# Kernel optimization log

Measured on AMD Instinct MI355X. Metric: run time of the kernel, lower is better.

## Reference

```python
import jax, jax.numpy as jnp
from jax import lax
import numpy as np

KS = 5
STRIDE = 4
SCALE = 10.0
PAD = 1        # conv_transpose2d padding (hardcoded in source)
OUT_PAD = 1    # output_padding
DN = ('NCHW', 'OIHW', 'NCHW')


def _same_pad(x, ks, stride):
    # torch same_padding: pad so out = ceil(H/stride)
    H, W = x.shape[-2], x.shape[-1]
    oh = -(-H // stride); ow = -(-W // stride)
    ph = max(0, (oh - 1) * stride + ks - H)
    pw = max(0, (ow - 1) * stride + ks - W)
    return jnp.pad(x, ((0, 0), (0, 0), (ph // 2, ph - ph // 2), (pw // 2, pw - pw // 2)))


def _patches(x, ks, stride):
    # torch extract_image_patches (same padding + unfold), returned as [N, L, C, ks, ks]
    N, C, H, W = x.shape
    oh = -(-H // stride); ow = -(-W // stride)
    xp = _same_pad(x, ks, stride)
    ys = (jnp.arange(oh) * stride)[:, None] + jnp.arange(ks)[None, :]   # [oh, ks]
    xs = (jnp.arange(ow) * stride)[:, None] + jnp.arange(ks)[None, :]   # [ow, ks]
    p = xp[:, :, ys, :][:, :, :, :, xs]   # [N, C, oh, ks, ow, ks]
    return p.transpose(0, 2, 4, 1, 3, 5).reshape(N, oh * ow, C, ks, ks)


def _conv3(x, W, b):
    # BasicBlock: 3x3 conv pad 1 + bias + LeakyReLU(0.01)
    y = lax.conv_general_dilated(x, W, (1, 1), [(1, 1), (1, 1)], dimension_numbers=DN)
    return jax.nn.leaky_relu(y + b[None, :, None, None], 0.01)


def _attend(qp, kp, vp):
    # qp: [C, Hp, Wp] padded query feature; kp: [L, C, ks, ks]; vp: [L, B, ks, ks]
    kmax = jnp.max(jnp.sqrt(jnp.sum(kp * kp, axis=(1, 2, 3))))
    kn = kp / kmax
    w = lax.conv_general_dilated(qp[None], kn, (STRIDE, STRIDE), 'VALID', dimension_numbers=DN)  # [1, L, h, w]
    wn = jax.nn.softmax(w * SCALE, axis=1)
    # conv_transpose2d(wn, vp, stride=4, padding=1, output_padding=1) as lhs-dilated conv
    ker = jnp.flip(vp.transpose(1, 0, 2, 3), (2, 3))  # [B, L, ks, ks]
    lo = KS - 1 - PAD
    hi = KS - 1 - PAD + OUT_PAD
    out = lax.conv_general_dilated(wn, ker, (1, 1), [(lo, hi), (lo, hi)],
                                   lhs_dilation=(STRIDE, STRIDE), dimension_numbers=DN)
    return out[0] / 6.0


def setup_inputs() -> dict:
    key = jax.random.key(0)
    k = jax.random.split(key, 12)
    N, CIN, MID, B = 8, 64, 64, 64
    H, HL = 256, 64
    s = 0.05
    return {
        'ms':   jax.random.normal(k[0], (N, B, HL, HL), jnp.float32),
        'pan':  jax.random.normal(k[1], (N, CIN, H, H), jnp.float32),
        'pan2': jax.random.normal(k[2], (N, CIN, HL, HL), jnp.float32),
        'Wq': jax.random.normal(k[3], (MID, CIN, 3, 3), jnp.float32) * s,
        'bq': jnp.zeros((MID,), jnp.float32),
        'Wk': jax.random.normal(k[4], (MID, CIN, 3, 3), jnp.float32) * s,
        'bk': jnp.zeros((MID,), jnp.float32),
        'Wv': jax.random.normal(k[5], (B, B, 3, 3), jnp.float32) * s,
        'bv': jnp.zeros((B,), jnp.float32),
        'Wr': jax.random.normal(k[6], (B, B, 3, 3), jnp.float32) * s,
        'br': jnp.zeros((B,), jnp.float32),
    }


def reference(ms, pan, pan2, Wq, bq, Wk, bk, Wv, bv, Wr, br):
    k_fea = _conv3(pan2, Wk, bk)               # [N, MID, 64, 64]
    k_patch = _patches(k_fea, KS, STRIDE)      # [N, L=256, MID, 5, 5]
    q_fea = _conv3(pan, Wq, bq)                # [N, MID, 256, 256]
    q_pad = _same_pad(q_fea, KS, STRIDE)       # [N, MID, 257, 257]
    v_fea = _conv3(ms, Wv, bv)                 # [N, B, 64, 64]
    v_patch = _patches(v_fea, KS, STRIDE)      # [N, L, B, 5, 5]
    res = jax.vmap(_attend)(q_pad, k_patch, v_patch)  # [N, B, 256, 256]
    return _conv3(res, Wr, br)
```

## Files before the change

### kernel.cpp

```cpp
#include <hip/hip_runtime.h>
#include <math.h>

#define NB   8
#define CI   64
#define COC  64
#define HQ   256
#define HK   64
#define KS   5
#define LL   256
#define NPAD 1664
#define QP2  (257 * 264)

typedef __attribute__((ext_vector_type(8))) short bf16x8s;
typedef __attribute__((ext_vector_type(4))) float f32x4;

static __device__ __forceinline__ unsigned short f2bf(float f) {
  union { float f; unsigned u; } v; v.f = f;
  unsigned r = v.u + 0x7FFF + ((v.u >> 16) & 1);
  return (unsigned short)(r >> 16);
}
static __device__ __forceinline__ float bf2f(unsigned short h) {
  union { unsigned u; float f; } v; v.u = ((unsigned)h) << 16; return v.f;
}

__global__ void wtrans_mfma(const float* __restrict__ Wt, unsigned short* __restrict__ wimg) {
  const int ch = blockIdx.x;
  const int tap = ch >> 1, cih = ch & 1;
  for (int idx = threadIdx.x; idx < 64 * 40; idx += 256) {
    const int co = idx / 40, s = idx - co * 40;
    unsigned short v = 0;
    if (s < 32) v = f2bf(Wt[((size_t)co * 64 + cih * 32 + s) * 9 + tap]);
    wimg[(size_t)ch * 64 * 40 + idx] = v;
  }
}

__global__ void pad_rci(const float* __restrict__ src, unsigned short* __restrict__ dst) {
  const int ct = blockIdx.x, g = blockIdx.y, n = blockIdx.z;
  const int c0 = ct * 66;
  __shared__ float t[64 * 68];
  const int jl = threadIdx.x & 63, cg = threadIdx.x >> 6;
  const int row = g - 1;
  const bool rok = (row >= 0 && row < 256);
  for (int ci = cg; ci < 64; ci += 4) {
    #pragma unroll
    for (int jb = 0; jb < 2; ++jb) {
      const int j = jl + jb * 64;
      if (j < 66) {
        const int x = c0 - 1 + j;
        float v = 0.f;
        if (rok && x >= 0 && x < 256)
          v = src[(((size_t)n * 64 + ci) * 256 + row) * 256 + x];
        t[ci * 68 + j] = v;
      }
    }
  }
  __syncthreads();
  const int cil = threadIdx.x & 63, cc = threadIdx.x >> 6;
  unsigned short* db = dst + (((size_t)n * 258 + g) * 264) * 64;
  for (int c = cc; c < 66; c += 4)
    db[(size_t)(c0 + c) * 64 + cil] = f2bf(t[cil * 68 + c]);
}

__global__ void pad_rci_s(const float* __restrict__ src, unsigned short* __restrict__ dst) {
  const int g = blockIdx.x;
  const int n = blockIdx.y;
  __shared__ float t[64 * 68];
  const int jl = threadIdx.x & 63, cg = threadIdx.x >> 6;
  const int row = g - 1;
  const bool rok = (row >= 0 && row < 64);
  for (int ci = cg; ci < 64; ci += 4) {
    #pragma unroll
    for (int jb = 0; jb < 2; ++jb) {
      const int j = jl + jb * 64;
      if (j < 66) {
        const int x = j - 1;
        float v = 0.f;
        if (rok && x >= 0 && x < 64)
          v = src[(((size_t)n * 64 + ci) * 64 + row) * 64 + x];
        t[ci * 68 + j] = v;
      }
    }
  }
  __syncthreads();
  const int cil = threadIdx.x & 63, cc = threadIdx.x >> 6;
  unsigned short* db = dst + ((size_t)n * 66 + g) * 72 * 64;
  for (int c = cc; c < 66; c += 4)
    db[(size_t)c * 64 + cil] = f2bf(t[cil * 68 + c]);
}

__global__ void rbz(unsigned short* __restrict__ resbf) {
  const int n = blockIdx.x;
  unsigned short* b = resbf + (size_t)n * 258 * 264 * 64;
  for (int idx = threadIdx.x; idx < 264 * 64; idx += 256) {
    b[idx] = 0;
    b[(size_t)257 * 264 * 64 + idx] = 0;
  }
  for (int idx = threadIdx.x; idx < 256 * 64; idx += 256) {
    const int r = idx >> 6, ci = idx & 63;
    b[((size_t)(r + 1) * 264) * 64 + ci] = 0;
    b[((size_t)(r + 1) * 264 + 257) * 64 + ci] = 0;
  }
}

__global__ void qz(unsigned short* __restrict__ qhi, unsigned short* __restrict__ qlo) {
  const int n = blockIdx.x;
  unsigned short* bh = qhi + (size_t)n * QP2 * 64;
  unsigned short* bl = qlo + (size_t)n * QP2 * 64;
  for (int g = threadIdx.x; g < 4224; g += 256) {
    ((unsigned long long*)(bh + (size_t)256 * 264 * 64))[g] = 0ull;
    ((unsigned long long*)(bl + (size_t)256 * 264 * 64))[g] = 0ull;
  }
  for (int g = threadIdx.x; g < 4096; g += 256) {
    const int r = g >> 4, q = g & 15;
    const size_t off = ((size_t)r * 264 + 256) * 64 + q * 4;
    *(unsigned long long*)(bh + off) = 0ull;
    *(unsigned long long*)(bl + off) = 0ull;
  }
}

__global__ __launch_bounds__(256) void conv3m(
    const unsigned short* __restrict__ inbf,
    const unsigned short* __restrict__ wimg,
    const float* __restrict__ bias,
    float* __restrict__ out, int PS, int RS, int inRS, long long inIS) {
  const int x0 = blockIdx.x * 64;
  const int y0 = blockIdx.y * 2;
  const int n  = blockIdx.z;
  const int tid = threadIdx.x;
  const int lane = tid & 63;
  const int wv = tid >> 6;
  const int col = lane & 15;
  const int kg  = lane >> 4;

  __shared__ unsigned short in_s[4 * 66 * 72];

  {
    const unsigned short* src = inbf + (size_t)n * inIS + (size_t)y0 * inRS;
    for (int pos = tid; pos < 264; pos += 256) {
      const int r = pos / 66, c = pos - r * 66;
      const unsigned short* s = src + (size_t)r * inRS + (size_t)(x0 + c) * 64;
      unsigned short* d = &in_s[pos * 72];
      #pragma unroll
      for (int q = 0; q < 8; ++q)
        *(float4*)(d + q * 8) = *(const float4*)(s + q * 8);
    }
  }
  __syncthreads();

  f32x4 acc[2][4];
  #pragma unroll
  for (int ry = 0; ry < 2; ++ry)
    #pragma unroll
    for (int p = 0; p < 4; ++p) acc[ry][p] = (f32x4){0.f, 0.f, 0.f, 0.f};

  const unsigned short* wbase = wimg + ((size_t)(wv * 16 + col)) * 40 + kg * 8;

  for (int ch = 0; ch < 18; ++ch) {
    const int tap = ch >> 1, cih = ch & 1;
    const int dy = tap / 3, dx = tap - dy * 3;
    const bf16x8s a = *(const bf16x8s*)(wbase + (size_t)ch * 64 * 40);
    const int cix = cih * 32 + kg * 8;
    #pragma unroll
    for (int ry = 0; ry < 2; ++ry)
      #pragma unroll
      for (int p = 0; p < 4; ++p) {
        const int c = p * 16 + col + dx;
        const bf16x8s b = *(const bf16x8s*)&in_s[((ry + dy) * 66 + c) * 72 + cix];
        acc[ry][p] = __builtin_amdgcn_mfma_f32_16x16x32_bf16(a, b, acc[ry][p], 0, 0, 0);
      }
  }

  const int cobase = wv * 16 + kg * 4;
  const float4 bb = *(const float4*)&bias[cobase];
  const float bv[4] = {bb.x, bb.y, bb.z, bb.w};
  #pragma unroll
  for (int ry = 0; ry < 2; ++ry)
    #pragma unroll
    for (int p = 0; p < 4; ++p) {
      const int x = x0 + p * 16 + col;
      #pragma unroll
      for (int r = 0; r < 4; ++r) {
        float t = acc[ry][p][r] + bv[r];
        t = t > 0.f ? t : 0.01f * t;
        out[(size_t)(n * 64 + cobase + r) * PS + (size_t)(y0 + ry) * RS + x] = t;
      }
    }
}

__global__ __launch_bounds__(256) void conv3mq(
    const unsigned short* __restrict__ inbf,
    const unsigned short* __restrict__ wimg,
    const float* __restrict__ bias,
    unsigned short* __restrict__ qhi, unsigned short* __restrict__ qlo) {
  const int x0 = blockIdx.x * 64;
  const int y0 = blockIdx.y * 2;
  const int n  = blockIdx.z;
  const int tid = threadIdx.x;
  const int lane = tid & 63;
  const int wv = tid >> 6;
  const int col = lane & 15;
  const int kg  = lane >> 4;

  __shared__ unsigned short in_s[4 * 66 * 72];

  {
    const unsigned short* src = inbf + ((size_t)n * 258 + y0) * 264 * 64;
    for (int pos = tid; pos < 264; pos += 256) {
      const int r = pos / 66, c = pos - r * 66;
      const unsigned short* s = src + ((size_t)r * 264 + x0 + c) * 64;
      unsigned short* d = &in_s[pos * 72];
      #pragma unroll
      for (int q = 0; q < 8; ++q)
        *(float4*)(d + q * 8) = *(const float4*)(s + q * 8);
    }
  }
  __syncthreads();

  f32x4 acc[2][4];
  #pragma unroll
  for (int ry = 0; ry < 2; ++ry)
    #pragma unroll
    for (int p = 0; p < 4; ++p) acc[ry][p] = (f32x4){0.f, 0.f, 0.f, 0.f};

  const unsigned short* wbase = wimg + ((size_t)(wv * 16 + col)) * 40 + kg * 8;

  for (int ch = 0; ch < 18; ++ch) {
    const int tap = ch >> 1, cih = ch & 1;
    const int dy = tap / 3, dx = tap - dy * 3;
    const bf16x8s a = *(const bf16x8s*)(wbase + (size_t)ch * 64 * 40);
    const int cix = cih * 32 + kg * 8;
    #pragma unroll
    for (int ry = 0; ry < 2; ++ry)
      #pragma unroll
      for (int p = 0; p < 4; ++p) {
        const int c = p * 16 + col + dx;
        const bf16x8s b = *(const bf16x8s*)&in_s[((ry + dy) * 66 + c) * 72 + cix];
        acc[ry][p] = __builtin_amdgcn_mfma_f32_16x16x32_bf16(a, b, acc[ry][p], 0, 0, 0);
      }
  }

  const int cobase = wv * 16 + kg * 4;
  const float4 bb = *(const float4*)&bias[cobase];
  const float bv[4] = {bb.x, bb.y, bb.z, bb.w};
  #pragma unroll
  for (int ry = 0; ry < 2; ++ry) {
    unsigned short* hb = qhi + ((size_t)n * 257 + (y0 + ry)) * 264 * 64;
    unsigned short* lb = qlo + ((size_t)n * 257 + (y0 + ry)) * 264 * 64;
    #pragma unroll
    for (int p = 0; p < 4; ++p) {
      const int x = x0 + p * 16 + col;
      unsigned long long hp = 0, lp = 0;
      #pragma unroll
      for (int r = 0; r < 4; ++r) {
        float t = acc[ry][p][r] + bv[r];
        t = t > 0.f ? t : 0.01f * t;
        const unsigned short h = f2bf(t);
        const unsigned short lo = f2bf(t - bf2f(h));
        hp |= ((unsigned long long)h) << (16 * r);
        lp |= ((unsigned long long)lo) << (16 * r);
      }
      *(unsigned long long*)(hb + (size_t)x * 64 + cobase) = hp;
      *(unsigned long long*)(lb + (size_t)x * 64 + cobase) = lp;
    }
  }
}

__global__ void knorm_kernel(const float* __restrict__ kfea, float* __restrict__ norms) {
  const int l = blockIdx.x, n = blockIdx.y, c = threadIdx.x;
  const int ly = l >> 4, lx = l & 15;
  const float* base = kfea + ((size_t)(n * CI + c) * HK) * HK;
  float ss = 0.f;
  #pragma unroll
  for (int i = 0; i < KS; ++i) {
    const int r = 4 * ly + i;
    if (r >= HK) continue;
    #pragma unroll
    for (int j = 0; j < KS; ++j) {
      const int cc = 4 * lx + j;
      if (cc >= HK) continue;
      const float v = base[r * HK + cc];
      ss = fmaf(v, v, ss);
    }
  }
  for (int off = 32; off; off >>= 1) ss += __shfl_down(ss, off);
  if (c == 0) norms[n * LL + l] = ss;
}

__global__ void kscale_kernel(const float* __restrict__ norms, float* __restrict__ kscale) {
  const int n = blockIdx.x, t = threadIdx.x;
  float v = norms[n * LL + t];
  for (int off = 32; off; off >>= 1) v = fmaxf(v, __shfl_down(v, off));
  __shared__ float red[4];
  if ((t & 63) == 0) red[t >> 6] = v;
  __syncthreads();
  if (t == 0) {
    const float m = fmaxf(fmaxf(red[0], red[1]), fmaxf(red[2], red[3]));
    kscale[n] = 10.0f / sqrtf(m);
  }
}

__global__ void kp_gather2(const float* __restrict__ kfea, const float* __restrict__ kscale,
                           unsigned short* __restrict__ khi, unsigned short* __restrict__ klo) {
  const int tap = blockIdx.x, cih = blockIdx.y, n = blockIdx.z;
  const int s = threadIdx.x & 31, lg = threadIdx.x >> 5;
  const int i = tap / 5, j = tap % 5;
  const float sc = kscale[n];
  const float* kb = kfea + ((size_t)(n * 64 + cih * 32 + s) * 64) * 64;
  const size_t ob = (((size_t)n * 50 + tap * 2 + cih) * 256) * 32;
  for (int lb = 0; lb < 32; ++lb) {
    const int l = lb * 8 + lg;
    const int r = 4 * (l >> 4) + i, c = 4 * (l & 15) + j;
    float v = 0.f;
    if (r < 64 && c < 64) v = kb[r * 64 + c] * sc;
    const unsigned short h = f2bf(v);
    khi[ob + (size_t)l * 32 + s] = h;
    klo[ob + (size_t)l * 32 + s] = f2bf(v - bf2f(h));
  }
}

__global__ __launch_bounds__(512) void qk_fused(
    const unsigned short* __restrict__ qhi, const unsigned short* __restrict__ qlo,
    const unsigned short* __restrict__ khi, const unsigned short* __restrict__ klo,
    unsigned short* __restrict__ wnbf) {
  const int yb = blockIdx.x, n = blockIdx.y;
  const int tid = threadIdx.x;
  const int lane = tid & 63, wv = tid >> 6;
  const int kh = wv >> 2, lq = wv & 3;
  const int col = lane & 15, kg = lane >> 4;

  __shared__ float sc_s[64 * 260];
  __shared__ float red[64][5];
  __shared__ float redm[64];

  f32x4 acc[4][4];
  #pragma unroll
  for (int fm = 0; fm < 4; ++fm)
    #pragma unroll
    for (int fn = 0; fn < 4; ++fn) acc[fm][fn] = (f32x4){0.f, 0.f, 0.f, 0.f};

  const unsigned short* khb = khi + (size_t)n * 50 * 8192;
  const unsigned short* klb = klo + (size_t)n * 50 * 8192;
  const unsigned short* qhb = qhi + (size_t)n * QP2 * 64;
  const unsigned short* qlb = qlo + (size_t)n * QP2 * 64;

  const int ch0 = kh * 25;
  for (int cc = 0; cc < 25; ++cc) {
    const int ch = ch0 + cc;
    const int tap = ch >> 1, cih = ch & 1;
    const int i = tap / 5, j = tap - 5 * i;
    bf16x8s ah[4], al[4];
    #pragma unroll
    for (int fm = 0; fm < 4; ++fm) {
      const size_t qoff = (((size_t)(4 * yb + i) * 264) + 4 * (fm * 16 + col) + j) * 64
                        + cih * 32 + kg * 8;
      ah[fm] = *(const bf16x8s*)(qhb + qoff);
      al[fm] = *(const bf16x8s*)(qlb + qoff);
    }
    #pragma unroll
    for (int fn = 0; fn < 4; ++fn) {
      const size_t boff = ((size_t)ch * 256 + lq * 64 + fn * 16 + col) * 32 + kg * 8;
      const bf16x8s bh = *(const bf16x8s*)(khb + boff);
      const bf16x8s bl = *(const bf16x8s*)(klb + boff);
      #pragma unroll
      for (int fm = 0; fm < 4; ++fm) {
        acc[fm][fn] = __builtin_amdgcn_mfma_f32_16x16x32_bf16(ah[fm], bh, acc[fm][fn], 0, 0, 0);
        acc[fm][fn] = __builtin_amdgcn_mfma_f32_16x16x32_bf16(ah[fm], bl, acc[fm][fn], 0, 0, 0);
        acc[fm][fn] = __builtin_amdgcn_mfma_f32_16x16x32_bf16(al[fm], bh, acc[fm][fn], 0, 0, 0);
      }
    }
  }

  if (kh == 1) {
    #pragma unroll
    for (int fm = 0; fm < 4; ++fm)
      #pragma unroll
      for (int fn = 0; fn < 4; ++fn)
        #pragma unroll
        for (int r = 0; r < 4; ++r)
          sc_s[(fm * 16 + kg * 4 + r) * 260 + lq * 64 + fn * 16 + col] = acc[fm][fn][r];
  }
  __syncthreads();
  if (kh == 0) {
    #pragma unroll
    for (int fm = 0; fm < 4; ++fm)
      #pragma unroll
      for (int fn = 0; fn < 4; ++fn)
        #pragma unroll
        for (int r = 0; r < 4; ++r)
          acc[fm][fn][r] += sc_s[(fm * 16 + kg * 4 + r) * 260 + lq * 64 + fn * 16 + col];

    #pragma unroll
    for (int fm = 0; fm < 4; ++fm)
      #pragma unroll
      for (int r = 0; r < 4; ++r) {
        float m = fmaxf(fmaxf(acc[fm][0][r], acc[fm][1][r]),
                        fmaxf(acc[fm][2][r], acc[fm][3][r]));
        #pragma unroll
        for (int off = 1; off < 16; off <<= 1) m = fmaxf(m, __shfl_xor(m, off));
        if (col == 0) red[fm * 16 + kg * 4 + r][lq] = m;
      }
  }
  __syncthreads();
  if (tid < 64) {
    redm[tid] = fmaxf(fmaxf(red[tid][0], red[tid][1]),
                      fmaxf(red[tid][2], red[tid][3]));
  }
  __syncthreads();
  if (kh == 0) {
    #pragma unroll
    for (int fm = 0; fm < 4; ++fm)
      #pragma unroll
      for (int r = 0; r < 4; ++r) {
        const float bm = redm[fm * 16 + kg * 4 + r];
        float s = 0.f;
        #pragma unroll
        for (int fn = 0; fn < 4; ++fn) {
          const float e = __expf(acc[fm][fn][r] - bm);
          acc[fm][fn][r] = e;
          s += e;
        }
        #pragma unroll
        for (int off = 1; off < 16; off <<= 1) s += __shfl_xor(s, off);
        if (col == 0) red[fm * 16 + kg * 4 + r][lq] = s;
      }
  }
  __syncthreads();
  if (tid < 64) {
    redm[tid] = 1.0f / (red[tid][0] + red[tid][1] + red[tid][2] + red[tid][3]);
  }
  __syncthreads();
  if (kh == 0) {
    unsigned short* wb = wnbf + ((size_t)n * 4096 + (size_t)yb * 64) * 256;
    #pragma unroll
    for (int fm = 0; fm < 4; ++fm)
      #pragma unroll
      for (int r = 0; r < 4; ++r) {
        const int q = fm * 16 + kg * 4 + r;
        const float inv = redm[q];
        #pragma unroll
        for (int fn = 0; fn < 4; ++fn)
          wb[(size_t)q * 256 + lq * 64 + fn * 16 + col] = f2bf(acc[fm][fn][r] * inv);
      }
  }
}

__global__ void vpt_gather(const float* __restrict__ vfea, unsigned short* __restrict__ vpt) {
  const int l4 = threadIdx.x & 63, bj = threadIdx.x >> 6;
  const int bij = blockIdx.x * 4 + bj;
  const int n = blockIdx.y;
  const int ij = bij >> 6, b = bij & 63;
  unsigned short o[4] = {0, 0, 0, 0};
  if (ij < 25) {
    const int i = ij / 5, j = ij % 5;
    const int ly = l4 >> 2;
    const int r = 4 * ly + i;
    if (r < HK) {
      const float* base = vfea + ((size_t)(n * COC + b) * HK + r) * HK;
      #pragma unroll
      for (int e = 0; e < 4; ++e) {
        const int lx = (l4 & 3) * 4 + e;
        const int c = 4 * lx + j;
        if (c < HK) o[e] = f2bf(base[c]);
      }
    }
  }
  unsigned long long pack = (unsigned long long)o[0] | ((unsigned long long)o[1] << 16)
                          | ((unsigned long long)o[2] << 32) | ((unsigned long long)o[3] << 48);
  *(unsigned long long*)(vpt + ((size_t)n * NPAD + bij) * 256 + l4 * 4) = pack;
}

__global__ __launch_bounds__(256) void pv_mfma(
    const unsigned short* __restrict__ wnb, const unsigned short* __restrict__ vpt,
    unsigned short* __restrict__ C0) {
  const int nz = blockIdx.z;
  const unsigned short* A = wnb + (size_t)nz * 4096 * 256;
  const unsigned short* B = vpt + (size_t)nz * NPAD * 256;
  unsigned short* C = C0 + (size_t)nz * 4096 * NPAD;
  const int m0 = blockIdx.x * 64;
  const int n0 = blockIdx.y * 128;
  const int tid = threadIdx.x;
  const int lane = tid & 63;
  const int wv = tid >> 6;
  const int wm = wv >> 1, wn_ = wv & 1;
  const int col = lane & 15, kg = lane >> 4;

  __shared__ unsigned short A_s[64 * 40];
  __shared__ unsigned short B_s[128 * 40];

  f32x4 acc[2][4];
  #pragma unroll
  for (int fm = 0; fm < 2; ++fm)
    #pragma unroll
    for (int fn = 0; fn < 4; ++fn) acc[fm][fn] = (f32x4){0.f, 0.f, 0.f, 0.f};

  for (int k0 = 0; k0 < 256; k0 += 32) {
    __syncthreads();
    {
      const int row = tid >> 2, q = tid & 3;
      *(float4*)&A_s[row * 40 + q * 8] =
          *(const float4*)&A[(size_t)(m0 + row) * 256 + k0 + q * 8];
    }
    {
      const int row = tid >> 1, hh = tid & 1;
      *(float4*)&B_s[row * 40 + hh * 16] =
          *(const float4*)&B[(size_t)(n0 + row) * 256 + k0 + hh * 16];
      *(float4*)&B_s[row * 40 + hh * 16 + 8] =
          *(const float4*)&B[(size_t)(n0 + row) * 256 + k0 + hh * 16 + 8];
    }
    __syncthreads();

    bf16x8s a[2], b[4];
    #pragma unroll
    for (int fm = 0; fm < 2; ++fm)
      a[fm] = *(const bf16x8s*)&A_s[(wm * 32 + fm * 16 + col) * 40 + kg * 8];
    #pragma unroll
    for (int fn = 0; fn < 4; ++fn)
      b[fn] = *(const bf16x8s*)&B_s[(wn_ * 64 + fn * 16 + col) * 40 + kg * 8];
    #pragma unroll
    for (int fm = 0; fm < 2; ++fm)
      #pragma unroll
      for (int fn = 0; fn < 4; ++fn)
        acc[fm][fn] = __builtin_amdgcn_mfma_f32_16x16x32_bf16(a[fm], b[fn], acc[fm][fn], 0, 0, 0);
  }

  #pragma unroll
  for (int fm = 0; fm < 2; ++fm) {
    #pragma unroll
    for (int fn = 0; fn < 4; ++fn) {
      const int cg = n0 + wn_ * 64 + fn * 16 + col;
      #pragma unroll
      for (int r = 0; r < 4; ++r) {
        const int rg = m0 + wm * 32 + fm * 16 + kg * 4 + r;
        C[(size_t)rg * NPAD + cg] = f2bf(acc[fm][fn][r]);
      }
    }
  }
}

__global__ __launch_bounds__(256) void u_scatter(
    const unsigned short* __restrict__ U0, unsigned short* __restrict__ resbf, int n0) {
  const int n = n0 + blockIdx.z;
  const unsigned short* U = U0 + (size_t)blockIdx.z * 4096 * NPAD;
  const int y = blockIdx.y;
  const int xt = blockIdx.x;
  const int tid = threadIdx.x;
  __shared__ float t_lds[64][65];
  const int ym = (y + 1) >> 2, yr = (y + 1) & 3;
  const bool v0 = (ym < 64);
  const bool v1 = (yr == 0 && ym >= 1);
  const int b = tid & 63, xg = tid >> 6;
  for (int xi = 0; xi < 16; ++xi) {
    const int x = xt * 64 + xg * 16 + xi;
    const int xm = (x + 1) >> 2, xr = (x + 1) & 3;
    const bool u0 = (xm < 64);
    const bool u1 = (xr == 0 && xm >= 1);
    float s = 0.f;
    if (v0) {
      const size_t rb = (size_t)(ym * 64) * NPAD;
      if (u0) s += bf2f(U[rb + (size_t)xm * NPAD + (yr * 5 + xr) * 64 + b]);
      if (u1) s += bf2f(U[rb + (size_t)(xm - 1) * NPAD + (yr * 5 + 4) * 64 + b]);
    }
    if (v1) {
      const size_t rb = (size_t)((ym - 1) * 64) * NPAD;
      if (u0) s += bf2f(U[rb + (size_t)xm * NPAD + (4 * 5 + xr) * 64 + b]);
      if (u1) s += bf2f(U[rb + (size_t)(xm - 1) * NPAD + (4 * 5 + 4) * 64 + b]);
    }
    t_lds[xg * 16 + xi][b] = s * (1.0f / 6.0f);
  }
  __syncthreads();
  unsigned short* db = resbf + (((size_t)n * 258 + (y + 1)) * 264) * 64;
  for (int xi = 0; xi < 16; ++xi) {
    const int x = xg * 16 + xi;
    db[(size_t)(xt * 64 + x + 1) * 64 + b] = f2bf(t_lds[x][b]);
  }
}

extern "C" void kernel_launch(void* const* d_in, const int* in_sizes, int n_in,
                              void* d_out, int out_size, void* d_ws, size_t ws_size,
                              hipStream_t stream) {
  const float* ms   = (const float*)d_in[0];
  const float* pan  = (const float*)d_in[1];
  const float* pan2 = (const float*)d_in[2];
  const float* Wq   = (const float*)d_in[3];
  const float* bq   = (const float*)d_in[4];
  const float* Wk   = (const float*)d_in[5];
  const float* bk   = (const float*)d_in[6];
  const float* Wv   = (const float*)d_in[7];
  const float* bv   = (const float*)d_in[8];
  const float* Wr   = (const float*)d_in[9];
  const float* br   = (const float*)d_in[10];
  float* out = (float*)d_out;

  float* ws = (float*)d_ws;
  const size_t SZ_QP  = (size_t)NB * CI * QP2;
  const size_t SZ_K   = (size_t)NB * CI * HK * HK;
  const size_t SZ_WN  = (size_t)NB * 64 * 64 * LL;
  const size_t SZ_VPT = (size_t)NB * NPAD * 256 / 2;
  const size_t SZ_KP  = (size_t)NB * 50 * 256 * 32;
  const size_t SZ_PS  = (size_t)NB * CI * 66 * 72;
  const size_t SZ_WI  = 23040;
  const size_t SZ_U1F = (size_t)4096 * NPAD / 2;
  const size_t SZ_UAF = (size_t)NB * SZ_U1F;

  float* q_pad   = ws;
  float* k_fea   = q_pad + SZ_QP;
  float* v_fea   = k_fea + SZ_K;
  float* wnbf_f  = v_fea + SZ_K;
  float* vptbf_f = wnbf_f + SZ_WN / 2;
  float* kp      = vptbf_f + SZ_VPT;
  float* norms   = kp + SZ_KP;
  float* kscale  = norms + NB * LL;
  float* wimgkf  = kscale + 64;
  float* wimgvf  = wimgkf + SZ_WI;
  float* wimgqf  = wimgvf + SZ_WI;
  float* wimgrf  = wimgqf + SZ_WI;
  float* msrci_f = wimgrf + SZ_WI;
  float* p2rci_f = msrci_f + SZ_PS;
  float* tail    = p2rci_f + SZ_PS;

  unsigned short* qhi  = (unsigned short*)q_pad;
  unsigned short* qlo  = qhi + (size_t)NB * QP2 * 64;
  unsigned short* khi  = (unsigned short*)kp;
  unsigned short* klo  = khi + (size_t)NB * 50 * 256 * 32;
  unsigned short* wimgk = (unsigned short*)wimgkf;
  unsigned short* wimgv = (unsigned short*)wimgvf;
  unsigned short* wimgq = (unsigned short*)wimgqf;
  unsigned short* wimgr = (unsigned short*)wimgrf;
  unsigned short* msrci = (unsigned short*)msrci_f;
  unsigned short* p2rci = (unsigned short*)p2rci_f;
  unsigned short* wnbf  = (unsigned short*)wnbf_f;
  unsigned short* vptbf = (unsigned short*)vptbf_f;
  unsigned short* panbf = (unsigned short*)tail;
  unsigned short* U     = (unsigned short*)tail;
  unsigned short* resbf = (unsigned short*)q_pad;

  const size_t base_elems = (size_t)(tail - ws);
  const bool batched = ws_size >= (base_elems + SZ_UAF) * sizeof(float);

  wtrans_mfma<<<dim3(18), 256, 0, stream>>>(Wk, wimgk);
  wtrans_mfma<<<dim3(18), 256, 0, stream>>>(Wv, wimgv);
  wtrans_mfma<<<dim3(18), 256, 0, stream>>>(Wq, wimgq);
  wtrans_mfma<<<dim3(18), 256, 0, stream>>>(Wr, wimgr);

  pad_rci_s<<<dim3(66, NB), 256, 0, stream>>>(ms, msrci);
  pad_rci_s<<<dim3(66, NB), 256, 0, stream>>>(pan2, p2rci);
  pad_rci<<<dim3(4, 258, NB), 256, 0, stream>>>(pan, panbf);

  conv3m<<<dim3(1, 32, NB), 256, 0, stream>>>(p2rci, wimgk, bk, k_fea, HK * HK, HK,
                                              72 * 64, (long long)66 * 72 * 64);
  conv3m<<<dim3(1, 32, NB), 256, 0, stream>>>(msrci, wimgv, bv, v_fea, HK * HK, HK,
                                              72 * 64, (long long)66 * 72 * 64);
  conv3mq<<<dim3(4, 128, NB), 256, 0, stream>>>(panbf, wimgq, bq, qhi, qlo);
  qz<<<dim3(NB), 256, 0, stream>>>(qhi, qlo);

  knorm_kernel<<<dim3(LL, NB), 64, 0, stream>>>(k_fea, norms);
  kscale_kernel<<<NB, 256, 0, stream>>>(norms, kscale);

  kp_gather2<<<dim3(25, 2, NB), 256, 0, stream>>>(k_fea, kscale, khi, klo);

  qk_fused<<<dim3(64, NB), 512, 0, stream>>>(qhi, qlo, khi, klo, wnbf);

  rbz<<<dim3(NB), 256, 0, stream>>>(resbf);

  vpt_gather<<<dim3(NPAD / 4, NB), 256, 0, stream>>>(v_fea, vptbf);

  if (batched) {
    pv_mfma<<<dim3(64, 13, NB), 256, 0, stream>>>(wnbf, vptbf, U);
    u_scatter<<<dim3(4, HQ, NB), 256, 0, stream>>>(U, resbf, 0);
  } else {
    for (int n = 0; n < NB; ++n) {
      pv_mfma<<<dim3(64, 13, 1), 256, 0, stream>>>(wnbf + (size_t)n * 4096 * 256,
                                                   vptbf + (size_t)n * NPAD * 256, U);
      u_scatter<<<dim3(4, HQ, 1), 256, 0, stream>>>(U, resbf, n);
    }
  }

  conv3m<<<dim3(4, 128, NB), 256, 0, stream>>>(resbf, wimgr, br, out, HQ * HQ, HQ,
                                               264 * 64, (long long)258 * 264 * 64);
}
```

Baseline: 662.6 us.

## Merge weight-transform and small-pad launches; drop LDS staging in pv_mfma

```diff
diff --git a/kernel.cpp b/kernel.cpp
--- a/kernel.cpp
+++ b/kernel.cpp
@@ -23,14 +23,18 @@
   union { unsigned u; float f; } v; v.u = ((unsigned)h) << 16; return v.f;
 }
 
-__global__ void wtrans_mfma(const float* __restrict__ Wt, unsigned short* __restrict__ wimg) {
-  const int ch = blockIdx.x;
+__global__ void wtrans_mfma4(const float* __restrict__ W0, const float* __restrict__ W1,
+                             const float* __restrict__ W2, const float* __restrict__ W3,
+                             unsigned short* __restrict__ wimg) {
+  const int ch = blockIdx.x, wsel = blockIdx.y;
+  const float* Wt = (wsel == 0) ? W0 : (wsel == 1) ? W1 : (wsel == 2) ? W2 : W3;
   const int tap = ch >> 1, cih = ch & 1;
+  unsigned short* dst = wimg + (size_t)wsel * 18 * 64 * 40 + (size_t)ch * 64 * 40;
   for (int idx = threadIdx.x; idx < 64 * 40; idx += 256) {
     const int co = idx / 40, s = idx - co * 40;
     unsigned short v = 0;
     if (s < 32) v = f2bf(Wt[((size_t)co * 64 + cih * 32 + s) * 9 + tap]);
-    wimg[(size_t)ch * 64 * 40 + idx] = v;
+    dst[idx] = v;
   }
 }
 
@@ -61,9 +65,13 @@
     db[(size_t)(c0 + c) * 64 + cil] = f2bf(t[cil * 68 + c]);
 }
 
-__global__ void pad_rci_s(const float* __restrict__ src, unsigned short* __restrict__ dst) {
+__global__ void pad_rci_s2(const float* __restrict__ s0, unsigned short* __restrict__ d0,
+                           const float* __restrict__ s1, unsigned short* __restrict__ d1) {
   const int g = blockIdx.x;
   const int n = blockIdx.y;
+  const int sel = blockIdx.z;
+  const float* src = sel ? s1 : s0;
+  unsigned short* dst = sel ? d1 : d0;
   __shared__ float t[64 * 68];
   const int jl = threadIdx.x & 63, cg = threadIdx.x >> 6;
   const int row = g - 1;
@@ -484,38 +492,23 @@
   const int wm = wv >> 1, wn_ = wv & 1;
   const int col = lane & 15, kg = lane >> 4;
 
-  __shared__ unsigned short A_s[64 * 40];
-  __shared__ unsigned short B_s[128 * 40];
-
   f32x4 acc[2][4];
   #pragma unroll
   for (int fm = 0; fm < 2; ++fm)
     #pragma unroll
     for (int fn = 0; fn < 4; ++fn) acc[fm][fn] = (f32x4){0.f, 0.f, 0.f, 0.f};
 
+  const unsigned short* Abase = A + (size_t)(m0 + wm * 32 + col) * 256 + kg * 8;
+  const unsigned short* Bbase = B + (size_t)(n0 + wn_ * 64 + col) * 256 + kg * 8;
+
   for (int k0 = 0; k0 < 256; k0 += 32) {
-    __syncthreads();
-    {
-      const int row = tid >> 2, q = tid & 3;
-      *(float4*)&A_s[row * 40 + q * 8] =
-          *(const float4*)&A[(size_t)(m0 + row) * 256 + k0 + q * 8];
-    }
-    {
-      const int row = tid >> 1, hh = tid & 1;
-      *(float4*)&B_s[row * 40 + hh * 16] =
-          *(const float4*)&B[(size_t)(n0 + row) * 256 + k0 + hh * 16];
-      *(float4*)&B_s[row * 40 + hh * 16 + 8] =
-          *(const float4*)&B[(size_t)(n0 + row) * 256 + k0 + hh * 16 + 8];
-    }
-    __syncthreads();
-
     bf16x8s a[2], b[4];
     #pragma unroll
     for (int fm = 0; fm < 2; ++fm)
-      a[fm] = *(const bf16x8s*)&A_s[(wm * 32 + fm * 16 + col) * 40 + kg * 8];
+      a[fm] = *(const bf16x8s*)(Abase + (size_t)(fm * 16) * 256 + k0);
     #pragma unroll
     for (int fn = 0; fn < 4; ++fn)
-      b[fn] = *(const bf16x8s*)&B_s[(wn_ * 64 + fn * 16 + col) * 40 + kg * 8];
+      b[fn] = *(const bf16x8s*)(Bbase + (size_t)(fn * 16) * 256 + k0);
     #pragma unroll
     for (int fm = 0; fm < 2; ++fm)
       #pragma unroll
@@ -598,7 +591,7 @@
   const size_t SZ_VPT = (size_t)NB * NPAD * 256 / 2;
   const size_t SZ_KP  = (size_t)NB * 50 * 256 * 32;
   const size_t SZ_PS  = (size_t)NB * CI * 66 * 72;
-  const size_t SZ_WI  = 23040;
+  const size_t SZ_WI4 = 4 * 23040;
   const size_t SZ_U1F = (size_t)4096 * NPAD / 2;
   const size_t SZ_UAF = (size_t)NB * SZ_U1F;
 
@@ -610,11 +603,8 @@
   float* kp      = vptbf_f + SZ_VPT;
   float* norms   = kp + SZ_KP;
   float* kscale  = norms + NB * LL;
-  float* wimgkf  = kscale + 64;
-  float* wimgvf  = wimgkf + SZ_WI;
-  float* wimgqf  = wimgvf + SZ_WI;
-  float* wimgrf  = wimgqf + SZ_WI;
-  float* msrci_f = wimgrf + SZ_WI;
+  float* wimgf   = kscale + 64;
+  float* msrci_f = wimgf + SZ_WI4;
   float* p2rci_f = msrci_f + SZ_PS;
   float* tail    = p2rci_f + SZ_PS;
 
@@ -622,10 +612,11 @@
   unsigned short* qlo  = qhi + (size_t)NB * QP2 * 64;
   unsigned short* khi  = (unsigned short*)kp;
   unsigned short* klo  = khi + (size_t)NB * 50 * 256 * 32;
-  unsigned short* wimgk = (unsigned short*)wimgkf;
-  unsigned short* wimgv = (unsigned short*)wimgvf;
-  unsigned short* wimgq = (unsigned short*)wimgqf;
-  unsigned short* wimgr = (unsigned short*)wimgrf;
+  unsigned short* wimg  = (unsigned short*)wimgf;
+  unsigned short* wimgk = wimg;
+  unsigned short* wimgv = wimg + (size_t)1 * 18 * 64 * 40;
+  unsigned short* wimgq = wimg + (size_t)2 * 18 * 64 * 40;
+  unsigned short* wimgr = wimg + (size_t)3 * 18 * 64 * 40;
   unsigned short* msrci = (unsigned short*)msrci_f;
   unsigned short* p2rci = (unsigned short*)p2rci_f;
   unsigned short* wnbf  = (unsigned short*)wnbf_f;
@@ -637,13 +628,9 @@
   const size_t base_elems = (size_t)(tail - ws);
   const bool batched = ws_size >= (base_elems + SZ_UAF) * sizeof(float);
 
-  wtrans_mfma<<<dim3(18), 256, 0, stream>>>(Wk, wimgk);
-  wtrans_mfma<<<dim3(18), 256, 0, stream>>>(Wv, wimgv);
-  wtrans_mfma<<<dim3(18), 256, 0, stream>>>(Wq, wimgq);
-  wtrans_mfma<<<dim3(18), 256, 0, stream>>>(Wr, wimgr);
-
-  pad_rci_s<<<dim3(66, NB), 256, 0, stream>>>(ms, msrci);
-  pad_rci_s<<<dim3(66, NB), 256, 0, stream>>>(pan2, p2rci);
+  wtrans_mfma4<<<dim3(18, 4), 256, 0, stream>>>(Wk, Wv, Wq, Wr, wimg);
+
+  pad_rci_s2<<<dim3(66, NB, 2), 256, 0, stream>>>(ms, msrci, pan2, p2rci);
   pad_rci<<<dim3(4, 258, NB), 256, 0, stream>>>(pan, panbf);
 
   conv3m<<<dim3(1, 32, NB), 256, 0, stream>>>(p2rci, wimgk, bk, k_fea, HK * HK, HK,
```

Measured after the change: 703.5 us. 6.2% more time.
